# Optimization experiments

Measured on AMD Instinct MI355X. Metric: run time of the kernel, lower is better.

## Reference

```python
import jax, jax.numpy as jnp
import numpy as np

# static config (matches init_kwargs)
B, H, W = 8, 64, 64
DIM, NH = 512, 16
HD = DIM // NH
WS = 8            # square window
SHIFT = 4
N = WS * WS       # tokens per window
NW = (H // WS) * (W // WS)  # windows per image
SCALE = HD ** (-0.5)
MLP_HIDDEN = int(DIM * 4.0)


def _rel_pos_index():
    coords = np.stack(np.meshgrid(np.arange(WS), np.arange(WS), indexing='ij'))  # [2,Wh,Ww]
    cf = coords.reshape(2, -1)
    rel = cf[:, :, None] - cf[:, None, :]          # [2,N,N]
    rel = rel.transpose(1, 2, 0)                    # [N,N,2]
    rel[:, :, 0] += WS - 1
    rel[:, :, 1] += WS - 1
    rel[:, :, 0] *= 2 * WS - 1
    return rel.sum(-1)                              # [N,N]

REL_IDX = jnp.asarray(_rel_pos_index())


def _attn_mask():
    img_mask = np.zeros((1, H, W, 1), np.float32)
    slices = (slice(0, -WS), slice(-WS, -SHIFT), slice(-SHIFT, None))
    cnt = 0
    for hs in slices:
        for ws in slices:
            img_mask[:, hs, ws, :] = cnt
            cnt += 1
    m = img_mask.reshape(1, H // WS, WS, W // WS, WS, 1).transpose(0, 1, 3, 2, 4, 5).reshape(-1, N)
    am = m[:, None, :] - m[:, :, None]
    return jnp.asarray(np.where(am != 0, -100.0, 0.0).astype(np.float32))  # [NW,N,N]

ATTN_MASK = _attn_mask()


def layernorm(x, g, b, eps=1e-5):
    mu = x.mean(-1, keepdims=True)
    var = ((x - mu) ** 2).mean(-1, keepdims=True)
    return (x - mu) * jax.lax.rsqrt(var + eps) * g + b


def setup_inputs() -> dict:
    key = jax.random.key(0)
    ks = jax.random.split(key, 12)
    s = 0.02
    return {
        'x': jax.random.normal(ks[0], (B, H * W, DIM), jnp.float32),
        'fundamental_context': jax.random.normal(ks[1], (B, 64), jnp.float32),
        'norm1_g': jnp.ones((DIM,), jnp.float32),
        'norm1_b': jnp.zeros((DIM,), jnp.float32),
        'qkv_w': jax.random.normal(ks[2], (DIM, 3 * DIM), jnp.float32) * s,
        'qkv_b': jnp.zeros((3 * DIM,), jnp.float32),
        'rel_bias_table': jax.random.normal(ks[3], ((2 * WS - 1) ** 2, NH), jnp.float32) * s,
        'proj_w': jax.random.normal(ks[4], (DIM, DIM), jnp.float32) * s,
        'proj_b': jnp.zeros((DIM,), jnp.float32),
        'norm2_g': jnp.ones((DIM,), jnp.float32),
        'norm2_b': jnp.zeros((DIM,), jnp.float32),
        'fc1_w': jax.random.normal(ks[5], (DIM, MLP_HIDDEN), jnp.float32) * s,
        'fc1_b': jnp.zeros((MLP_HIDDEN,), jnp.float32),
        'fc2_w': jax.random.normal(ks[6], (MLP_HIDDEN, DIM), jnp.float32) * s,
        'fc2_b': jnp.zeros((DIM,), jnp.float32),
    }


def reference(x, fundamental_context, norm1_g, norm1_b, qkv_w, qkv_b,
              rel_bias_table, proj_w, proj_b, norm2_g, norm2_b,
              fc1_w, fc1_b, fc2_w, fc2_b):
    shortcut = x
    h = layernorm(x, norm1_g, norm1_b).reshape(B, H, W, DIM)
    # cyclic shift (SW-MSA)
    h = jnp.roll(h, (-SHIFT, -SHIFT), axis=(1, 2))
    # window partition -> [B*NW, N, C]
    win = h.reshape(B, H // WS, WS, W // WS, WS, DIM).transpose(0, 1, 3, 2, 4, 5)
    win = win.reshape(B * NW, N, DIM)
    # windowed multi-head attention
    qkv = (win @ qkv_w + qkv_b).reshape(B * NW, N, 3, NH, HD).transpose(2, 0, 3, 1, 4)
    q, k, v = qkv[0] * SCALE, qkv[1], qkv[2]          # [B_,NH,N,HD]
    attn = jnp.einsum('bhnd,bhmd->bhnm', q, k)        # [B_,NH,N,N]
    bias = rel_bias_table[REL_IDX.reshape(-1)].reshape(N, N, NH).transpose(2, 0, 1)
    attn = attn + bias[None]
    attn = attn.reshape(B, NW, NH, N, N) + ATTN_MASK[None, :, None]
    attn = jax.nn.softmax(attn.reshape(B * NW, NH, N, N), axis=-1)
    out = jnp.einsum('bhnm,bhmd->bhnd', attn, v).transpose(0, 2, 1, 3).reshape(B * NW, N, DIM)
    out = out @ proj_w + proj_b
    # window reverse -> [B,H,W,C]
    out = out.reshape(B, H // WS, W // WS, WS, WS, DIM).transpose(0, 1, 3, 2, 4, 5).reshape(B, H, W, DIM)
    # reverse cyclic shift
    out = jnp.roll(out, (SHIFT, SHIFT), axis=(1, 2)).reshape(B, H * W, DIM)
    x = shortcut + out
    # MLP block
    h = layernorm(x, norm2_g, norm2_b)
    h = jax.nn.gelu(h @ fc1_w + fc1_b, approximate=False) @ fc2_w + fc2_b
    return x + h
```

## Files before the change

kernel.cpp:

```cpp
#include <hip/hip_runtime.h>
#include <cstddef>
#include <cstdint>


typedef unsigned short u16;
typedef __attribute__((ext_vector_type(8))) short short8;
typedef __attribute__((ext_vector_type(4))) float floatx4;

__device__ __forceinline__ float bf2f(u16 u) {
    union { float f; unsigned i; } w; w.i = ((unsigned)u) << 16; return w.f;
}
__device__ __forceinline__ u16 f2bf(float f) {
    union { float f; unsigned i; } w; w.f = f;
    unsigned r = w.i + 0x7FFF + ((w.i >> 16) & 1);
    return (u16)(r >> 16);
}

__device__ __forceinline__ void gload_lds16(const u16* g, u16* l) {
    __builtin_amdgcn_global_load_lds(
        (const __attribute__((address_space(1))) void*)g,
        (__attribute__((address_space(3))) void*)l, 16, 0, 0);
}

__device__ __forceinline__ float erf_fast(float x) {
    float ax = fabsf(x);
    float t = 1.0f / (1.0f + 0.3275911f * ax);
    float poly = ((((1.061405429f * t - 1.453152027f) * t + 1.421413741f) * t
                   - 0.284496736f) * t + 0.254829592f) * t;
    float er = 1.0f - poly * __expf(-ax * ax);
    return copysignf(er, x);
}

__device__ __forceinline__ int win_to_img_row(int t) {
    int win = t >> 6, n = t & 63;
    int b = win >> 6, wr = (win >> 3) & 7, wc = win & 7;
    int h = ((wr << 3) + (n >> 3) + 4) & 63;
    int w = ((wc << 3) + (n & 7) + 4) & 63;
    return (b << 12) + (h << 6) + w;
}

__global__ __launch_bounds__(256) void ln_fused(
    const float* __restrict__ x, const float* __restrict__ g,
    const float* __restrict__ b, u16* __restrict__ out, int gather)
{
    int wave = threadIdx.x >> 6, lane = threadIdx.x & 63;
    int t = blockIdx.x * 4 + wave;
    int src = gather ? win_to_img_row(t) : t;
    const float* xr = x + (size_t)src * 512 + lane * 8;
    float4 a = *(const float4*)xr;
    float4 c = *(const float4*)(xr + 4);
    float s = a.x + a.y + a.z + a.w + c.x + c.y + c.z + c.w;
    float s2 = a.x*a.x + a.y*a.y + a.z*a.z + a.w*a.w
             + c.x*c.x + c.y*c.y + c.z*c.z + c.w*c.w;
#pragma unroll
    for (int off = 32; off; off >>= 1) { s += __shfl_down(s, off); s2 += __shfl_down(s2, off); }
    s = __shfl(s, 0); s2 = __shfl(s2, 0);
    float mu = s * (1.f / 512.f);
    float var = s2 * (1.f / 512.f) - mu * mu;
    float rs = rsqrtf(var + 1e-5f);
    int col = lane * 8;
    float4 g0 = *(const float4*)(g + col), g1 = *(const float4*)(g + col + 4);
    float4 b0 = *(const float4*)(b + col), b1 = *(const float4*)(b + col + 4);
    u16 r[8];
    r[0] = f2bf((a.x - mu) * rs * g0.x + b0.x);
    r[1] = f2bf((a.y - mu) * rs * g0.y + b0.y);
    r[2] = f2bf((a.z - mu) * rs * g0.z + b0.z);
    r[3] = f2bf((a.w - mu) * rs * g0.w + b0.w);
    r[4] = f2bf((c.x - mu) * rs * g1.x + b1.x);
    r[5] = f2bf((c.y - mu) * rs * g1.y + b1.y);
    r[6] = f2bf((c.z - mu) * rs * g1.z + b1.z);
    r[7] = f2bf((c.w - mu) * rs * g1.w + b1.w);
    *(uint4*)(out + (size_t)t * 512 + col) = *(const uint4*)r;
}

__global__ __launch_bounds__(256) void transpose_k(
    const float* __restrict__ W, u16* __restrict__ WT, int K, int N)
{
    int f = blockIdx.x * 256 + threadIdx.x;
    int n = f % N, kc = f / N;
    if (kc >= (K >> 3)) return;
    int k0 = kc << 3;
    u16 r[8];
#pragma unroll
    for (int j = 0; j < 8; ++j) r[j] = f2bf(W[(size_t)(k0 + j) * N + n]);
    *(uint4*)(WT + (size_t)n * K + k0) = *(const uint4*)r;
}

enum { M_QKV = 0, M_PROJ = 1, M_GELU = 2, M_FINAL = 3 };

template <int MODE, int ASRC>
__global__ __launch_bounds__(256, 4) void gemm_bt(
    const u16* __restrict__ A, int lda,
    const u16* __restrict__ BT, int ldb,
    const float* __restrict__ bias,
    void* __restrict__ outp, const float* __restrict__ auxf, int K)
{
    __shared__ __align__(16) u16 As[128 * 64];
    __shared__ __align__(16) u16 Bs[128 * 64];

    int tid = threadIdx.x;
    int nwg = gridDim.x * gridDim.y;
    int bid = blockIdx.y * gridDim.x + blockIdx.x;
    int q8 = nwg >> 3, r8 = nwg & 7;
    int xcd = bid & 7, pos = bid >> 3;
    int swz = (xcd < r8 ? xcd * (q8 + 1)
                        : r8 * (q8 + 1) + (xcd - r8) * q8) + pos;
    int bx = swz % gridDim.x, by = swz / gridDim.x;
    int bm = by * 128, bn = bx * 128;

    int wave = tid >> 6, lane = tid & 63;
    int quad = lane >> 4, lr = lane & 15;
    int wm = (wave >> 1) * 64, wn = (wave & 1) * 64;

    floatx4 acc[4][4] = {};

    for (int k0 = 0; k0 < K; k0 += 64) {
#pragma unroll
        for (int l = 0; l < 4; ++l) {
            int f = (l << 8) + tid;
            int row = f >> 3, c = f & 7;
            int cs = c ^ (row & 7);
            int kk = k0 + (cs << 3);
            const u16* gb = BT + (size_t)(bn + row) * ldb + kk;
            gload_lds16(gb, Bs + f * 8);
            if constexpr (ASRC == 0) {
                gload_lds16(A + (size_t)(bm + row) * lda + kk, As + f * 8);
            } else {
                int m = bm + row;
                gload_lds16(A + (size_t)(((m >> 6) << 4) + (kk >> 5)) * 2048
                              + (m & 63) * 32 + (kk & 31), As + f * 8);
            }
        }
        __syncthreads();
#pragma unroll
        for (int step = 0; step < 2; ++step) {
            short8 af[4], bv[4];
            int kc = step * 4 + quad;
#pragma unroll
            for (int t = 0; t < 4; ++t) {
                int ra = wm + t * 16 + lr;
                int rb = wn + t * 16 + lr;
                af[t] = *(const short8*)(As + ra * 64 + ((kc ^ (ra & 7)) << 3));
                bv[t] = *(const short8*)(Bs + rb * 64 + ((kc ^ (rb & 7)) << 3));
            }
#pragma unroll
            for (int mt = 0; mt < 4; ++mt)
#pragma unroll
                for (int nt = 0; nt < 4; ++nt)
                    acc[mt][nt] = __builtin_amdgcn_mfma_f32_16x16x32_bf16(
                        af[mt], bv[nt], acc[mt][nt], 0, 0, 0);
        }
        __syncthreads();
    }

#pragma unroll
    for (int mt = 0; mt < 4; ++mt) {
#pragma unroll
        for (int nt = 0; nt < 4; ++nt) {
            int m0 = bm + wm + mt * 16 + quad * 4;
            int n = bn + wn + nt * 16 + lr;
#pragma unroll
            for (int i = 0; i < 4; ++i) {
                int m = m0 + i;
                float v = acc[mt][nt][i];
                if constexpr (MODE == M_QKV) {
                    v += bias[n];
                    int sel = n >> 9, head = (n >> 5) & 15, d = n & 31;
                    int wh = (m >> 6) * 16 + head, tok = m & 63;
                    ((u16*)outp)[(size_t)sel * 16777216 + (size_t)wh * 2048 + tok * 32 + d] = f2bf(v);
                } else if constexpr (MODE == M_PROJ) {
                    size_t idx = (size_t)win_to_img_row(m) * 512 + n;
                    ((float*)outp)[idx] = v + bias[n] + auxf[idx];
                } else if constexpr (MODE == M_GELU) {
                    v += bias[n];
                    float gel = 0.5f * v * (1.0f + erf_fast(v * 0.70710678118654752f));
                    ((u16*)outp)[(size_t)m * 2048 + n] = f2bf(gel);
                } else {
                    size_t idx = (size_t)m * 512 + n;
                    float* o = (float*)outp;
                    o[idx] = o[idx] + v + bias[n];
                }
            }
        }
    }
}

__global__ __launch_bounds__(256) void attn_mfma(
    const u16* __restrict__ qkv, const float* __restrict__ table,
    u16* __restrict__ outp)
{
    __shared__ __align__(8) u16 PT[4][64 * 76];
    __shared__ float blds[225];

    int w = threadIdx.x >> 6, lane = threadIdx.x & 63;
    int head = blockIdx.x & 15, win = ((blockIdx.x >> 4) << 2) + w;
    int wh = (win << 4) + head;
    int quad = lane >> 4, lr = lane & 15;
    const u16* qb = qkv + (size_t)wh * 2048;
    const u16* kb = qb + 16777216;
    const u16* vb = qb + 33554432;
    u16* PTw = PT[w];

    for (int i = threadIdx.x; i < 225; i += 256) blds[i] = table[i * 16 + head];
    __syncthreads();

    short8 qf[4], kf[4];
#pragma unroll
    for (int t = 0; t < 4; ++t) {
        qf[t] = *(const short8*)(qb + (t * 16 + lr) * 32 + quad * 8);
        kf[t] = *(const short8*)(kb + (t * 16 + lr) * 32 + quad * 8);
    }
    floatx4 s[4][4] = {};
#pragma unroll
    for (int mi = 0; mi < 4; ++mi)
#pragma unroll
        for (int ni = 0; ni < 4; ++ni)
            s[mi][ni] = __builtin_amdgcn_mfma_f32_16x16x32_bf16(qf[mi], kf[ni], s[mi][ni], 0, 0, 0);

    short8 vf[2][2];
#pragma unroll
    for (int ks = 0; ks < 2; ++ks)
#pragma unroll
        for (int nd = 0; nd < 2; ++nd)
#pragma unroll
            for (int j = 0; j < 8; ++j)
                vf[ks][nd][j] = (short)vb[(ks * 32 + quad * 8 + j) * 32 + nd * 16 + lr];

    int wr = (win >> 3) & 7, wc = win & 7;
    int rj[4], cj[4], regj[4];
#pragma unroll
    for (int ni = 0; ni < 4; ++ni) {
        int kj = ni * 16 + lr;
        rj[ni] = kj >> 3; cj[ni] = kj & 7;
        int hJ = wr * 8 + rj[ni], wJ = wc * 8 + cj[ni];
        regj[ni] = (hJ < 56 ? 0 : (hJ < 60 ? 1 : 2)) * 3 + (wJ < 56 ? 0 : (wJ < 60 ? 1 : 2));
    }
    float rm[4][4], linv[4][4];
#pragma unroll
    for (int mi = 0; mi < 4; ++mi) {
#pragma unroll
        for (int i = 0; i < 4; ++i) {
            int qi = mi * 16 + quad * 4 + i;
            int ri = qi >> 3, ci = qi & 7;
            int hI = wr * 8 + ri, wI = wc * 8 + ci;
            int regi = (hI < 56 ? 0 : (hI < 60 ? 1 : 2)) * 3 + (wI < 56 ? 0 : (wI < 60 ? 1 : 2));
            float mx = -1e30f;
#pragma unroll
            for (int ni = 0; ni < 4; ++ni) {
                float v = s[mi][ni][i] * 0.17677669529663687f
                        + blds[(ri - rj[ni] + 7) * 15 + (ci - cj[ni] + 7)];
                if (regj[ni] != regi) v -= 100.f;
                s[mi][ni][i] = v;
                mx = fmaxf(mx, v);
            }
            rm[mi][i] = mx;
        }
    }
#pragma unroll
    for (int mi = 0; mi < 4; ++mi)
#pragma unroll
        for (int i = 0; i < 4; ++i) {
            float mx = rm[mi][i];
#pragma unroll
            for (int msk = 1; msk < 16; msk <<= 1) mx = fmaxf(mx, __shfl_xor(mx, msk));
            float sum = 0.f;
#pragma unroll
            for (int ni = 0; ni < 4; ++ni) {
                float e = __expf(s[mi][ni][i] - mx);
                s[mi][ni][i] = e;
                sum += e;
            }
#pragma unroll
            for (int msk = 1; msk < 16; msk <<= 1) sum += __shfl_xor(sum, msk);
            linv[mi][i] = 1.f / sum;
        }

#pragma unroll
    for (int mi = 0; mi < 4; ++mi)
#pragma unroll
        for (int ni = 0; ni < 4; ++ni) {
            unsigned lo = (unsigned)f2bf(s[mi][ni][0]) | ((unsigned)f2bf(s[mi][ni][1]) << 16);
            unsigned hi = (unsigned)f2bf(s[mi][ni][2]) | ((unsigned)f2bf(s[mi][ni][3]) << 16);
            uint2 pk = make_uint2(lo, hi);
            *(uint2*)(PTw + (ni * 16 + lr) * 76 + mi * 16 + quad * 4) = pk;
        }
    __syncthreads();

    floatx4 o[4][2] = {};
#pragma unroll
    for (int mi = 0; mi < 4; ++mi) {
#pragma unroll
        for (int ks = 0; ks < 2; ++ks) {
            short8 pa;
#pragma unroll
            for (int j = 0; j < 8; ++j)
                pa[j] = (short)PTw[(ks * 32 + quad * 8 + j) * 76 + mi * 16 + lr];
#pragma unroll
            for (int nd = 0; nd < 2; ++nd)
                o[mi][nd] = __builtin_amdgcn_mfma_f32_16x16x32_bf16(pa, vf[ks][nd], o[mi][nd], 0, 0, 0);
        }
    }
    u16* ob = outp + (size_t)wh * 2048;
#pragma unroll
    for (int mi = 0; mi < 4; ++mi)
#pragma unroll
        for (int nd = 0; nd < 2; ++nd)
#pragma unroll
            for (int i = 0; i < 4; ++i) {
                int qi = mi * 16 + quad * 4 + i;
                ob[qi * 32 + nd * 16 + lr] = f2bf(o[mi][nd][i] * linv[mi][i]);
            }
}

extern "C" void kernel_launch(void* const* d_in, const int* in_sizes, int n_in,
                              void* d_out, int out_size, void* d_ws, size_t ws_size,
                              hipStream_t stream)
{
    (void)in_sizes; (void)n_in; (void)out_size; (void)ws_size;
    const float* x      = (const float*)d_in[0];
    const float* n1g    = (const float*)d_in[2];
    const float* n1b    = (const float*)d_in[3];
    const float* qkv_w  = (const float*)d_in[4];
    const float* qkv_b  = (const float*)d_in[5];
    const float* table  = (const float*)d_in[6];
    const float* proj_w = (const float*)d_in[7];
    const float* proj_b = (const float*)d_in[8];
    const float* n2g    = (const float*)d_in[9];
    const float* n2b    = (const float*)d_in[10];
    const float* fc1_w  = (const float*)d_in[11];
    const float* fc1_b  = (const float*)d_in[12];
    const float* fc2_w  = (const float*)d_in[13];
    const float* fc2_b  = (const float*)d_in[14];
    float* out = (float*)d_out;
    char* ws = (char*)d_ws;

    u16* qkvT  = (u16*)ws;
    u16* projT = qkvT + 786432;
    u16* fc1T  = projT + 262144;
    u16* fc2T  = fc1T + 1048576;
    u16* q    = (u16*)(ws + 8388608);
    u16* h2   = q;
    u16* gbuf = q + 16777216;
    u16* xw   = (u16*)d_out;

    transpose_k<<<384, 256, 0, stream>>>(qkv_w, qkvT, 512, 1536);
    transpose_k<<<128, 256, 0, stream>>>(proj_w, projT, 512, 512);
    transpose_k<<<512, 256, 0, stream>>>(fc1_w, fc1T, 512, 2048);
    transpose_k<<<512, 256, 0, stream>>>(fc2_w, fc2T, 2048, 512);

    ln_fused<<<8192, 256, 0, stream>>>(x, n1g, n1b, xw, 1);
    gemm_bt<M_QKV, 0><<<dim3(12, 256), 256, 0, stream>>>(
        xw, 512, qkvT, 512, qkv_b, q, nullptr, 512);
    attn_mfma<<<2048, 256, 0, stream>>>(q, table, q);
    gemm_bt<M_PROJ, 3><<<dim3(4, 256), 256, 0, stream>>>(
        q, 0, projT, 512, proj_b, out, x, 512);
    ln_fused<<<8192, 256, 0, stream>>>(out, n2g, n2b, h2, 0);
    for (int mc = 0; mc < 2; ++mc) {
        gemm_bt<M_GELU, 0><<<dim3(16, 128), 256, 0, stream>>>(
            h2 + (size_t)mc * 16384 * 512, 512, fc1T, 512, fc1_b,
            gbuf, nullptr, 512);
        gemm_bt<M_FINAL, 0><<<dim3(4, 128), 256, 0, stream>>>(
            gbuf, 2048, fc2T, 2048, fc2_b,
            out + (size_t)mc * 16384 * 512, nullptr, 2048);
    }
}
```

Before: 500.3 us.

## Use 256x128 GEMM tiles with 3-stage LDS ring pipeline

Replaces the 128x128 single-buffered GEMM with a 512-thread kernel that computes 256x128 tiles. Global-to-LDS loads are prefetched two K-steps ahead through a triple-buffered ring, with explicit vmcnt waits so loads overlap the MFMA work. MFMA sections get raised wave priority. This aims to hide memory latency and to reuse each B tile across more rows, at the cost of 144KB of LDS per block, which allows only one block per CU.

Result: no change. 503.8 us (+0.7%).

```diff
diff --git a/kernel.cpp b/kernel.cpp
--- a/kernel.cpp
+++ b/kernel.cpp
@@ -20,6 +20,17 @@
     __builtin_amdgcn_global_load_lds(
         (const __attribute__((address_space(1))) void*)g,
         (__attribute__((address_space(3))) void*)l, 16, 0, 0);
+}
+
+__device__ __forceinline__ void ring_bar6() {
+    __builtin_amdgcn_sched_barrier(0);
+    asm volatile("s_waitcnt vmcnt(6) lgkmcnt(0)\n\ts_barrier" ::: "memory");
+    __builtin_amdgcn_sched_barrier(0);
+}
+__device__ __forceinline__ void ring_bar0() {
+    __builtin_amdgcn_sched_barrier(0);
+    asm volatile("s_waitcnt vmcnt(0) lgkmcnt(0)\n\ts_barrier" ::: "memory");
+    __builtin_amdgcn_sched_barrier(0);
 }
 
 __device__ __forceinline__ float erf_fast(float x) {
@@ -89,14 +100,13 @@
 enum { M_QKV = 0, M_PROJ = 1, M_GELU = 2, M_FINAL = 3 };
 
 template <int MODE, int ASRC>
-__global__ __launch_bounds__(256, 4) void gemm_bt(
+__global__ __launch_bounds__(512, 1) void gemm256(
     const u16* __restrict__ A, int lda,
     const u16* __restrict__ BT, int ldb,
     const float* __restrict__ bias,
     void* __restrict__ outp, const float* __restrict__ auxf, int K)
 {
-    __shared__ __align__(16) u16 As[128 * 64];
-    __shared__ __align__(16) u16 Bs[128 * 64];
+    __shared__ __align__(16) u16 lds[3 * 24576];
 
     int tid = threadIdx.x;
     int nwg = gridDim.x * gridDim.y;
@@ -106,63 +116,88 @@
     int swz = (xcd < r8 ? xcd * (q8 + 1)
                         : r8 * (q8 + 1) + (xcd - r8) * q8) + pos;
     int bx = swz % gridDim.x, by = swz / gridDim.x;
-    int bm = by * 128, bn = bx * 128;
+    int bm = by * 256, bn = bx * 128;
 
     int wave = tid >> 6, lane = tid & 63;
     int quad = lane >> 4, lr = lane & 15;
     int wm = (wave >> 1) * 64, wn = (wave & 1) * 64;
 
     floatx4 acc[4][4] = {};
-
-    for (int k0 = 0; k0 < K; k0 += 64) {
+    int nt = K >> 6;
+
+    auto stage = [&](int t) {
+        u16* slot = lds + (t % 3) * 24576;
+        int k0 = t << 6;
 #pragma unroll
         for (int l = 0; l < 4; ++l) {
-            int f = (l << 8) + tid;
+            int f = (l << 9) + tid;
             int row = f >> 3, c = f & 7;
-            int cs = c ^ (row & 7);
-            int kk = k0 + (cs << 3);
-            const u16* gb = BT + (size_t)(bn + row) * ldb + kk;
-            gload_lds16(gb, Bs + f * 8);
+            int kk = k0 + ((c ^ (row & 7)) << 3);
             if constexpr (ASRC == 0) {
-                gload_lds16(A + (size_t)(bm + row) * lda + kk, As + f * 8);
+                gload_lds16(A + (size_t)(bm + row) * lda + kk, slot + f * 8);
             } else {
                 int m = bm + row;
                 gload_lds16(A + (size_t)(((m >> 6) << 4) + (kk >> 5)) * 2048
-                              + (m & 63) * 32 + (kk & 31), As + f * 8);
-            }
-        }
-        __syncthreads();
+                              + (m & 63) * 32 + (kk & 31), slot + f * 8);
+            }
+        }
+#pragma unroll
+        for (int l = 0; l < 2; ++l) {
+            int f = (l << 9) + tid;
+            int row = f >> 3, c = f & 7;
+            int kk = k0 + ((c ^ (row & 7)) << 3);
+            gload_lds16(BT + (size_t)(bn + row) * ldb + kk,
+                        slot + 16384 + f * 8);
+        }
+    };
+
+    auto compute = [&](int t) {
+        const u16* As = lds + (t % 3) * 24576;
+        const u16* Bs = As + 16384;
 #pragma unroll
         for (int step = 0; step < 2; ++step) {
             short8 af[4], bv[4];
             int kc = step * 4 + quad;
 #pragma unroll
-            for (int t = 0; t < 4; ++t) {
-                int ra = wm + t * 16 + lr;
-                int rb = wn + t * 16 + lr;
-                af[t] = *(const short8*)(As + ra * 64 + ((kc ^ (ra & 7)) << 3));
-                bv[t] = *(const short8*)(Bs + rb * 64 + ((kc ^ (rb & 7)) << 3));
-            }
+            for (int tt = 0; tt < 4; ++tt) {
+                int ra = wm + tt * 16 + lr;
+                int rb = wn + tt * 16 + lr;
+                af[tt] = *(const short8*)(As + ra * 64 + ((kc ^ (ra & 7)) << 3));
+                bv[tt] = *(const short8*)(Bs + rb * 64 + ((kc ^ (rb & 7)) << 3));
+            }
+            __builtin_amdgcn_s_setprio(1);
 #pragma unroll
             for (int mt = 0; mt < 4; ++mt)
 #pragma unroll
-                for (int nt = 0; nt < 4; ++nt)
-                    acc[mt][nt] = __builtin_amdgcn_mfma_f32_16x16x32_bf16(
-                        af[mt], bv[nt], acc[mt][nt], 0, 0, 0);
-        }
-        __syncthreads();
-    }
+                for (int nn = 0; nn < 4; ++nn)
+                    acc[mt][nn] = __builtin_amdgcn_mfma_f32_16x16x32_bf16(
+                        af[mt], bv[nn], acc[mt][nn], 0, 0, 0);
+            __builtin_amdgcn_s_setprio(0);
+        }
+    };
+
+    stage(0);
+    stage(1);
+    ring_bar6();
+    for (int t = 0; t + 2 < nt; ++t) {
+        stage(t + 2);
+        compute(t);
+        ring_bar6();
+    }
+    compute(nt - 2);
+    ring_bar0();
+    compute(nt - 1);
 
 #pragma unroll
     for (int mt = 0; mt < 4; ++mt) {
 #pragma unroll
-        for (int nt = 0; nt < 4; ++nt) {
+        for (int nn = 0; nn < 4; ++nn) {
             int m0 = bm + wm + mt * 16 + quad * 4;
-            int n = bn + wn + nt * 16 + lr;
+            int n = bn + wn + nn * 16 + lr;
 #pragma unroll
             for (int i = 0; i < 4; ++i) {
                 int m = m0 + i;
-                float v = acc[mt][nt][i];
+                float v = acc[mt][nn][i];
                 if constexpr (MODE == M_QKV) {
                     v += bias[n];
                     int sel = n >> 9, head = (n >> 5) & 15, d = n & 31;
@@ -349,17 +384,17 @@
     transpose_k<<<512, 256, 0, stream>>>(fc2_w, fc2T, 2048, 512);
 
     ln_fused<<<8192, 256, 0, stream>>>(x, n1g, n1b, xw, 1);
-    gemm_bt<M_QKV, 0><<<dim3(12, 256), 256, 0, stream>>>(
+    gemm256<M_QKV, 0><<<dim3(12, 128), 512, 0, stream>>>(
         xw, 512, qkvT, 512, qkv_b, q, nullptr, 512);
     attn_mfma<<<2048, 256, 0, stream>>>(q, table, q);
-    gemm_bt<M_PROJ, 3><<<dim3(4, 256), 256, 0, stream>>>(
+    gemm256<M_PROJ, 3><<<dim3(4, 128), 512, 0, stream>>>(
         q, 0, projT, 512, proj_b, out, x, 512);
     ln_fused<<<8192, 256, 0, stream>>>(out, n2g, n2b, h2, 0);
     for (int mc = 0; mc < 2; ++mc) {
-        gemm_bt<M_GELU, 0><<<dim3(16, 128), 256, 0, stream>>>(
+        gemm256<M_GELU, 0><<<dim3(16, 64), 512, 0, stream>>>(
             h2 + (size_t)mc * 16384 * 512, 512, fc1T, 512, fc1_b,
             gbuf, nullptr, 512);
-        gemm_bt<M_FINAL, 0><<<dim3(4, 128), 256, 0, stream>>>(
+        gemm256<M_FINAL, 0><<<dim3(4, 64), 512, 0, stream>>>(
             gbuf, 2048, fc2T, 2048, fc2_b,
             out + (size_t)mc * 16384 * 512, nullptr, 2048);
     }
```

## Split MLP over hidden dimension instead of tokens and merge weight transposes

Applied to the files above, without the earlier changes.

The MLP is now chunked along the hidden dimension (two halves of 1024) over all tokens, instead of along the token dimension with the full 2048 hidden width. Each fc2 pass accumulates a partial K=1024 product into the output, and the bias is added only on the first pass. The four weight-transpose launches are also merged into one kernel with block-range dispatch to cut launch overhead. The fc2 grids double in size, but each pass re-reads and rewrites the full fp32 output, adding memory traffic.

Measured after the change: 510.1 us. About the same (+2.0%).

```diff
diff --git a/kernel.cpp b/kernel.cpp
--- a/kernel.cpp
+++ b/kernel.cpp
@@ -73,10 +73,19 @@
     *(uint4*)(out + (size_t)t * 512 + col) = *(const uint4*)r;
 }
 
-__global__ __launch_bounds__(256) void transpose_k(
-    const float* __restrict__ W, u16* __restrict__ WT, int K, int N)
-{
-    int f = blockIdx.x * 256 + threadIdx.x;
+__global__ __launch_bounds__(256) void transpose_all(
+    const float* __restrict__ qkv_w, const float* __restrict__ proj_w,
+    const float* __restrict__ fc1_w, const float* __restrict__ fc2_w,
+    u16* __restrict__ qkvT, u16* __restrict__ projT,
+    u16* __restrict__ fc1T, u16* __restrict__ fc2T)
+{
+    int bid = blockIdx.x;
+    const float* W; u16* WT; int K, N, base;
+    if (bid < 384)       { W = qkv_w;  WT = qkvT;  K = 512;  N = 1536; base = 0; }
+    else if (bid < 512)  { W = proj_w; WT = projT; K = 512;  N = 512;  base = 384; }
+    else if (bid < 1024) { W = fc1_w;  WT = fc1T;  K = 512;  N = 2048; base = 512; }
+    else                 { W = fc2_w;  WT = fc2T;  K = 2048; N = 512;  base = 1024; }
+    int f = (bid - base) * 256 + threadIdx.x;
     int n = f % N, kc = f / N;
     if (kc >= (K >> 3)) return;
     int k0 = kc << 3;
@@ -93,7 +102,7 @@
     const u16* __restrict__ A, int lda,
     const u16* __restrict__ BT, int ldb,
     const float* __restrict__ bias,
-    void* __restrict__ outp, const float* __restrict__ auxf, int K)
+    void* __restrict__ outp, const float* __restrict__ auxf, int K, int ldo)
 {
     __shared__ __align__(16) u16 As[128 * 64];
     __shared__ __align__(16) u16 Bs[128 * 64];
@@ -174,11 +183,12 @@
                 } else if constexpr (MODE == M_GELU) {
                     v += bias[n];
                     float gel = 0.5f * v * (1.0f + erf_fast(v * 0.70710678118654752f));
-                    ((u16*)outp)[(size_t)m * 2048 + n] = f2bf(gel);
+                    ((u16*)outp)[(size_t)m * ldo + n] = f2bf(gel);
                 } else {
                     size_t idx = (size_t)m * 512 + n;
                     float* o = (float*)outp;
-                    o[idx] = o[idx] + v + bias[n];
+                    float bb = bias ? bias[n] : 0.0f;
+                    o[idx] = o[idx] + v + bb;
                 }
             }
         }
@@ -343,24 +353,22 @@
     u16* gbuf = q + 16777216;
     u16* xw   = (u16*)d_out;
 
-    transpose_k<<<384, 256, 0, stream>>>(qkv_w, qkvT, 512, 1536);
-    transpose_k<<<128, 256, 0, stream>>>(proj_w, projT, 512, 512);
-    transpose_k<<<512, 256, 0, stream>>>(fc1_w, fc1T, 512, 2048);
-    transpose_k<<<512, 256, 0, stream>>>(fc2_w, fc2T, 2048, 512);
+    transpose_all<<<1536, 256, 0, stream>>>(
+        qkv_w, proj_w, fc1_w, fc2_w, qkvT, projT, fc1T, fc2T);
 
     ln_fused<<<8192, 256, 0, stream>>>(x, n1g, n1b, xw, 1);
     gemm_bt<M_QKV, 0><<<dim3(12, 256), 256, 0, stream>>>(
-        xw, 512, qkvT, 512, qkv_b, q, nullptr, 512);
+        xw, 512, qkvT, 512, qkv_b, q, nullptr, 512, 0);
     attn_mfma<<<2048, 256, 0, stream>>>(q, table, q);
     gemm_bt<M_PROJ, 3><<<dim3(4, 256), 256, 0, stream>>>(
-        q, 0, projT, 512, proj_b, out, x, 512);
+        q, 0, projT, 512, proj_b, out, x, 512, 0);
     ln_fused<<<8192, 256, 0, stream>>>(out, n2g, n2b, h2, 0);
-    for (int mc = 0; mc < 2; ++mc) {
-        gemm_bt<M_GELU, 0><<<dim3(16, 128), 256, 0, stream>>>(
-            h2 + (size_t)mc * 16384 * 512, 512, fc1T, 512, fc1_b,
-            gbuf, nullptr, 512);
-        gemm_bt<M_FINAL, 0><<<dim3(4, 128), 256, 0, stream>>>(
-            gbuf, 2048, fc2T, 2048, fc2_b,
-            out + (size_t)mc * 16384 * 512, nullptr, 2048);
-    }
-}
+    for (int nc = 0; nc < 2; ++nc) {
+        gemm_bt<M_GELU, 0><<<dim3(8, 256), 256, 0, stream>>>(
+            h2, 512, fc1T + (size_t)nc * 1024 * 512, 512,
+            fc1_b + nc * 1024, gbuf, nullptr, 512, 1024);
+        gemm_bt<M_FINAL, 0><<<dim3(4, 256), 256, 0, stream>>>(
+            gbuf, 1024, fc2T + nc * 1024, 2048,
+            (nc == 0 ? fc2_b : nullptr), out, nullptr, 1024, 0);
+    }
+}
```
